# Kernel tuning notes

Measured on AMD Instinct MI355X. Metric: run time of the kernel, lower is better.

## Reference

```python
import jax, jax.numpy as jnp
import numpy as np

N, IN_CH, HID, N_CLS = 12000, 256, 64, 40
EDGE_PROB = 0.002  # ~24 avg degree


def setup_inputs() -> dict:
    key = jax.random.key(0)
    k = jax.random.split(key, 5)
    x = jax.random.normal(k[0], (N, IN_CH), dtype=jnp.float32)
    adj = (jax.random.uniform(k[1], (N, N), dtype=jnp.float32) < EDGE_PROB).astype(jnp.float32)
    W_in = jax.random.normal(k[2], (IN_CH, HID), dtype=jnp.float32) * 0.05
    b_in = jnp.zeros((HID,), dtype=jnp.float32)
    W_cls = jax.random.normal(k[3], (HID, N_CLS), dtype=jnp.float32) * 0.05
    b_cls = jnp.zeros((N_CLS,), dtype=jnp.float32)
    return {"x": x, "adj": adj, "W_in": W_in, "b_in": b_in, "W_cls": W_cls, "b_cls": b_cls}


def reference(x, adj, W_in, b_in, W_cls, b_cls):
    # fc_in projection (always applied in AllGNN.forward)
    h = x @ W_in + b_in                         # [N, HID]
    # calc_degree(adj).unsqueeze(-1): row-sum degree reduction
    deg = jnp.sum(adj, axis=1, keepdims=True)   # [N, 1]
    # degree-informed classifier: mean-style neighborhood aggregation + linear head
    agg = (adj @ h) / (deg + 1.0)               # [N, HID]
    out = agg @ W_cls + b_cls                   # [N, N_CLS]
    return out
```

## Files before the change

kernel.cpp:

```cpp
#include <hip/hip_runtime.h>


#define NN     12000
#define INCH   256
#define HID    64
#define NCLS   40
#define NCHUNK ((NN + 255) / 256)
#define CAP    512

typedef float f4 __attribute__((ext_vector_type(4)));

__global__ __launch_bounds__(256) void fc_in_kernel(
    const float* __restrict__ x, const float* __restrict__ W_in,
    const float* __restrict__ b_in, float* __restrict__ h)
{
    const int lane = threadIdx.x & 63;
    const int w    = threadIdx.x >> 6;
    int rbase = (blockIdx.x * 4 + w) * 4;
    rbase = __builtin_amdgcn_readfirstlane(rbase);

    const float* __restrict__ xr = x + (size_t)rbase * INCH;
    const float  b = b_in[lane];
    float acc0 = b, acc1 = b, acc2 = b, acc3 = b;

    #pragma unroll 8
    for (int c = 0; c < INCH; ++c) {
        float wv = W_in[c * HID + lane];
        acc0 = fmaf(xr[c],            wv, acc0);
        acc1 = fmaf(xr[INCH + c],     wv, acc1);
        acc2 = fmaf(xr[2 * INCH + c], wv, acc2);
        acc3 = fmaf(xr[3 * INCH + c], wv, acc3);
    }
    float* hp = h + (size_t)rbase * HID + lane;
    hp[0 * HID] = acc0;
    hp[1 * HID] = acc1;
    hp[2 * HID] = acc2;
    hp[3 * HID] = acc3;
}

__global__ __launch_bounds__(256) void gnn_agg_kernel(
    const float* __restrict__ adj, const float* __restrict__ h,
    const float* __restrict__ W_cls, const float* __restrict__ b_cls,
    float* __restrict__ out)
{
    const int lane = threadIdx.x & 63;
    const int w    = threadIdx.x >> 6;
    const int row  = blockIdx.x;

    __shared__ int   s_cnt[4];
    __shared__ int   s_col[4][CAP];
    __shared__ float s_val[4][CAP];
    __shared__ float s_acc[4][HID];
    __shared__ float s_deg[4];

    if (lane == 0) s_cnt[w] = 0;

    const float* __restrict__ arow = adj + (size_t)row * NN;
    const int bl = lane * 4;
    float deg = 0.0f;

    auto loadc = [&](int ci) -> f4 {
        const int base = ci * 256 + bl;
        f4 v = {0.f, 0.f, 0.f, 0.f};
        if (base + 4 <= NN)
            v = __builtin_nontemporal_load(reinterpret_cast<const f4*>(arow + base));
        return v;
    };
    auto scan = [&](f4 v, int ci) {
        deg += (v[0] + v[1]) + (v[2] + v[3]);
        const int col = ci * 256 + bl;
        #pragma unroll
        for (int i = 0; i < 4; ++i) {
            if (v[i] != 0.0f) {
                int idx = atomicAdd(&s_cnt[w], 1);
                if (idx < CAP) { s_col[w][idx] = col + i; s_val[w][idx] = v[i]; }
            }
        }
    };

    for (int c = w; c < NCHUNK; c += 16) {
        f4 v0 = loadc(c);
        f4 v1 = (c + 4  < NCHUNK) ? loadc(c + 4)  : f4{0.f, 0.f, 0.f, 0.f};
        f4 v2 = (c + 8  < NCHUNK) ? loadc(c + 8)  : f4{0.f, 0.f, 0.f, 0.f};
        f4 v3 = (c + 12 < NCHUNK) ? loadc(c + 12) : f4{0.f, 0.f, 0.f, 0.f};
        scan(v0, c);
        scan(v1, c + 4);
        scan(v2, c + 8);
        scan(v3, c + 12);
    }

    float acc = 0.0f;
    int n = s_cnt[w];
    n = (n < CAP) ? n : CAP;
    int i = 0;
    for (; i + 4 <= n; i += 4) {
        int   c0 = s_col[w][i],     c1 = s_col[w][i + 1];
        int   c2 = s_col[w][i + 2], c3 = s_col[w][i + 3];
        float a0 = s_val[w][i],     a1 = s_val[w][i + 1];
        float a2 = s_val[w][i + 2], a3 = s_val[w][i + 3];
        float h0 = h[(size_t)c0 * HID + lane];
        float h1 = h[(size_t)c1 * HID + lane];
        float h2 = h[(size_t)c2 * HID + lane];
        float h3 = h[(size_t)c3 * HID + lane];
        acc = fmaf(a0, h0, fmaf(a1, h1, fmaf(a2, h2, fmaf(a3, h3, acc))));
    }
    for (; i < n; ++i)
        acc = fmaf(s_val[w][i], h[(size_t)s_col[w][i] * HID + lane], acc);

    #pragma unroll
    for (int off = 32; off; off >>= 1) deg += __shfl_xor(deg, off);
    s_acc[w][lane] = acc;
    if (lane == 0) s_deg[w] = deg;
    __syncthreads();

    if (w == 0) {
        float a  = (s_acc[0][lane] + s_acc[1][lane])
                 + (s_acc[2][lane] + s_acc[3][lane]);
        float dt = (s_deg[0] + s_deg[1]) + (s_deg[2] + s_deg[3]);
        float agg = a * __frcp_rn(dt + 1.0f);

        const int cl = (lane < NCLS) ? lane : 0;
        float o = b_cls[cl];
        #pragma unroll 8
        for (int k = 0; k < HID; ++k) {
            float av = __shfl(agg, k);
            o = fmaf(av, W_cls[k * NCLS + cl], o);
        }
        if (lane < NCLS) out[(size_t)row * NCLS + lane] = o;
    }
}

extern "C" void kernel_launch(void* const* d_in, const int* in_sizes, int n_in,
                              void* d_out, int out_size, void* d_ws, size_t ws_size,
                              hipStream_t stream)
{
    const float* x     = (const float*)d_in[0];
    const float* adj   = (const float*)d_in[1];
    const float* W_in  = (const float*)d_in[2];
    const float* b_in  = (const float*)d_in[3];
    const float* W_cls = (const float*)d_in[4];
    const float* b_cls = (const float*)d_in[5];
    float* out = (float*)d_out;
    float* h   = (float*)d_ws;

    fc_in_kernel<<<NN / 16, 256, 0, stream>>>(x, W_in, b_in, h);
    gnn_agg_kernel<<<NN, 256, 0, stream>>>(adj, h, W_cls, b_cls, out);
}
```

Before: 114.9 us.

## Fold W_in·W_cls into one projection and aggregate 40-wide features

Measured after the change: 124.9 us. +8.7%, slower.

```diff
diff --git a/kernel.cpp b/kernel.cpp
--- a/kernel.cpp
+++ b/kernel.cpp
@@ -6,42 +6,73 @@
 #define HID    64
 #define NCLS   40
 #define NCHUNK ((NN + 255) / 256)
-#define CAP    512
+#define CAP    64
 
 typedef float f4 __attribute__((ext_vector_type(4)));
 
-__global__ __launch_bounds__(256) void fc_in_kernel(
-    const float* __restrict__ x, const float* __restrict__ W_in,
-    const float* __restrict__ b_in, float* __restrict__ h)
+__global__ __launch_bounds__(256) void prep_kernel(
+    const float* __restrict__ W_in, const float* __restrict__ b_in,
+    const float* __restrict__ W_cls, float* __restrict__ Wc,
+    float* __restrict__ bc)
+{
+    const int r  = threadIdx.x;
+    const int c0 = blockIdx.x * 4;
+    float a0 = 0.f, a1 = 0.f, a2 = 0.f, a3 = 0.f;
+    #pragma unroll 8
+    for (int k = 0; k < HID; ++k) {
+        float w = W_in[r * HID + k];
+        const float* wc = W_cls + k * NCLS + c0;
+        a0 = fmaf(w, wc[0], a0);
+        a1 = fmaf(w, wc[1], a1);
+        a2 = fmaf(w, wc[2], a2);
+        a3 = fmaf(w, wc[3], a3);
+    }
+    float* o = Wc + r * NCLS + c0;
+    o[0] = a0; o[1] = a1; o[2] = a2; o[3] = a3;
+
+    if (blockIdx.x == 0 && r < NCLS) {
+        float s = 0.f;
+        #pragma unroll 8
+        for (int k = 0; k < HID; ++k)
+            s = fmaf(b_in[k], W_cls[k * NCLS + r], s);
+        bc[r] = s;
+    }
+}
+
+__global__ __launch_bounds__(256) void g_kernel(
+    const float* __restrict__ x, const float* __restrict__ Wc,
+    const float* __restrict__ bc, float* __restrict__ g)
 {
     const int lane = threadIdx.x & 63;
     const int w    = threadIdx.x >> 6;
     int rbase = (blockIdx.x * 4 + w) * 4;
     rbase = __builtin_amdgcn_readfirstlane(rbase);
 
+    const int cl = (lane < NCLS) ? lane : NCLS - 1;
     const float* __restrict__ xr = x + (size_t)rbase * INCH;
-    const float  b = b_in[lane];
+    const float b = bc[cl];
     float acc0 = b, acc1 = b, acc2 = b, acc3 = b;
 
     #pragma unroll 8
     for (int c = 0; c < INCH; ++c) {
-        float wv = W_in[c * HID + lane];
+        float wv = Wc[c * NCLS + cl];
         acc0 = fmaf(xr[c],            wv, acc0);
         acc1 = fmaf(xr[INCH + c],     wv, acc1);
         acc2 = fmaf(xr[2 * INCH + c], wv, acc2);
         acc3 = fmaf(xr[3 * INCH + c], wv, acc3);
     }
-    float* hp = h + (size_t)rbase * HID + lane;
-    hp[0 * HID] = acc0;
-    hp[1 * HID] = acc1;
-    hp[2 * HID] = acc2;
-    hp[3 * HID] = acc3;
+    if (lane < NCLS) {
+        float* gp = g + (size_t)rbase * NCLS + lane;
+        gp[0 * NCLS] = acc0;
+        gp[1 * NCLS] = acc1;
+        gp[2 * NCLS] = acc2;
+        gp[3 * NCLS] = acc3;
+    }
 }
 
 __global__ __launch_bounds__(256) void gnn_agg_kernel(
-    const float* __restrict__ adj, const float* __restrict__ h,
-    const float* __restrict__ W_cls, const float* __restrict__ b_cls,
-    float* __restrict__ out)
+    const float* __restrict__ adj, const float* __restrict__ g,
+    const float* __restrict__ b_cls, float* __restrict__ out)
 {
     const int lane = threadIdx.x & 63;
     const int w    = threadIdx.x >> 6;
@@ -50,7 +81,7 @@
     __shared__ int   s_cnt[4];
     __shared__ int   s_col[4][CAP];
     __shared__ float s_val[4][CAP];
-    __shared__ float s_acc[4][HID];
+    __shared__ float s_acc[4][64];
     __shared__ float s_deg[4];
 
     if (lane == 0) s_cnt[w] = 0;
@@ -67,13 +98,16 @@
         return v;
     };
     auto scan = [&](f4 v, int ci) {
-        deg += (v[0] + v[1]) + (v[2] + v[3]);
-        const int col = ci * 256 + bl;
-        #pragma unroll
-        for (int i = 0; i < 4; ++i) {
-            if (v[i] != 0.0f) {
-                int idx = atomicAdd(&s_cnt[w], 1);
-                if (idx < CAP) { s_col[w][idx] = col + i; s_val[w][idx] = v[i]; }
+        float s = (v[0] + v[1]) + (v[2] + v[3]);
+        deg += s;
+        if (__any(s != 0.0f)) {
+            const int col = ci * 256 + bl;
+            #pragma unroll
+            for (int i = 0; i < 4; ++i) {
+                if (v[i] != 0.0f) {
+                    int idx = atomicAdd(&s_cnt[w], 1);
+                    if (idx < CAP) { s_col[w][idx] = col + i; s_val[w][idx] = v[i]; }
+                }
             }
         }
     };
@@ -89,6 +123,7 @@
         scan(v3, c + 12);
     }
 
+    const int cl = (lane < NCLS) ? lane : NCLS - 1;
     float acc = 0.0f;
     int n = s_cnt[w];
     n = (n < CAP) ? n : CAP;
@@ -98,14 +133,14 @@
         int   c2 = s_col[w][i + 2], c3 = s_col[w][i + 3];
         float a0 = s_val[w][i],     a1 = s_val[w][i + 1];
         float a2 = s_val[w][i + 2], a3 = s_val[w][i + 3];
-        float h0 = h[(size_t)c0 * HID + lane];
-        float h1 = h[(size_t)c1 * HID + lane];
-        float h2 = h[(size_t)c2 * HID + lane];
-        float h3 = h[(size_t)c3 * HID + lane];
-        acc = fmaf(a0, h0, fmaf(a1, h1, fmaf(a2, h2, fmaf(a3, h3, acc))));
+        float g0 = g[(size_t)c0 * NCLS + cl];
+        float g1 = g[(size_t)c1 * NCLS + cl];
+        float g2 = g[(size_t)c2 * NCLS + cl];
+        float g3 = g[(size_t)c3 * NCLS + cl];
+        acc = fmaf(a0, g0, fmaf(a1, g1, fmaf(a2, g2, fmaf(a3, g3, acc))));
     }
     for (; i < n; ++i)
-        acc = fmaf(s_val[w][i], h[(size_t)s_col[w][i] * HID + lane], acc);
+        acc = fmaf(s_val[w][i], g[(size_t)s_col[w][i] * NCLS + cl], acc);
 
     #pragma unroll
     for (int off = 32; off; off >>= 1) deg += __shfl_xor(deg, off);
@@ -113,20 +148,11 @@
     if (lane == 0) s_deg[w] = deg;
     __syncthreads();
 
-    if (w == 0) {
+    if (w == 0 && lane < NCLS) {
         float a  = (s_acc[0][lane] + s_acc[1][lane])
                  + (s_acc[2][lane] + s_acc[3][lane]);
         float dt = (s_deg[0] + s_deg[1]) + (s_deg[2] + s_deg[3]);
-        float agg = a * __frcp_rn(dt + 1.0f);
-
-        const int cl = (lane < NCLS) ? lane : 0;
-        float o = b_cls[cl];
-        #pragma unroll 8
-        for (int k = 0; k < HID; ++k) {
-            float av = __shfl(agg, k);
-            o = fmaf(av, W_cls[k * NCLS + cl], o);
-        }
-        if (lane < NCLS) out[(size_t)row * NCLS + lane] = o;
+        out[(size_t)row * NCLS + lane] = a * __frcp_rn(dt + 1.0f) + b_cls[lane];
     }
 }
 
@@ -141,8 +167,12 @@
     const float* W_cls = (const float*)d_in[4];
     const float* b_cls = (const float*)d_in[5];
     float* out = (float*)d_out;
-    float* h   = (float*)d_ws;
 
-    fc_in_kernel<<<NN / 16, 256, 0, stream>>>(x, W_in, b_in, h);
-    gnn_agg_kernel<<<NN, 256, 0, stream>>>(adj, h, W_cls, b_cls, out);
+    float* g  = (float*)d_ws;
+    float* Wc = g + (size_t)NN * NCLS;
+    float* bc = Wc + INCH * NCLS;
+
+    prep_kernel<<<NCLS / 4, 256, 0, stream>>>(W_in, b_in, W_cls, Wc, bc);
+    g_kernel<<<NN / 16, 256, 0, stream>>>(x, Wc, bc, g);
+    gnn_agg_kernel<<<NN, 256, 0, stream>>>(adj, g, b_cls, out);
 }
```
